# Kernel tuning notes

Measured on AMD Instinct MI355X. Metric: run time of the kernel, lower is better.

The kernel has to match this reference:

```python
import jax, jax.numpy as jnp
import numpy as np

B, S, N, D = 32, 512, 64, 64


def setup_inputs() -> dict:
    key = jax.random.key(0)
    ks = jax.random.split(key, 6)
    return {
        "x": jax.random.normal(ks[0], (B, S, N, D), dtype=jnp.float32),
        "q_embed_weight": jax.random.normal(ks[1], (N, D), dtype=jnp.float32) * 0.02,
        "Wq_w": jax.random.normal(ks[2], (D, D), dtype=jnp.float32) * (1.0 / np.sqrt(D)),
        "Wq_b": jax.random.normal(ks[3], (D,), dtype=jnp.float32) * 0.02,
        "Wkv_w": jax.random.normal(ks[4], (2 * D, D), dtype=jnp.float32) * (1.0 / np.sqrt(D)),
        "Wkv_b": jax.random.normal(ks[5], (2 * D,), dtype=jnp.float32) * 0.02,
    }


def reference(x, q_embed_weight, Wq_w, Wq_b, Wkv_w, Wkv_b):
    d = x.shape[-1]
    # q = Wq(q_embed.weight): [n, d]
    q = q_embed_weight @ Wq_w.T + Wq_b
    # Wkv(x) -> [b, s, n, 2d]; chunk -> k is first half (v half is computed but unused, matching torch)
    kv = jnp.einsum('bsnd,ed->bsne', x, Wkv_w) + Wkv_b
    k = kv[..., :d]
    # prod: full contraction over n and d -> [b, s]
    prod = jnp.einsum('nd,bsnd->bs', q, k) / jnp.sqrt(jnp.asarray(d, x.dtype))
    attn = jax.nn.softmax(prod, axis=1)  # softmax over s
    # weighted sum over s with v = x (original overwrites v): [b, n, d]
    out = jnp.einsum('bs,bsnd->bnd', attn, x)
    return out
```

## Files before the change

kernel.cpp:

```cpp
#include <hip/hip_runtime.h>

#define B_    32
#define S_    512
#define ND_   4096
#define ND4_  1024
#define SCH   16
#define CH    32
#define NPH   (CH/2)
#define NUNIT (B_ * SCH)

typedef float f4 __attribute__((ext_vector_type(4)));
typedef float f2 __attribute__((ext_vector_type(2)));

__global__ void qw_kernel(const float* __restrict__ qe, const float* __restrict__ Wq_w,
                          const float* __restrict__ Wq_b, const float* __restrict__ Wkv_w,
                          float* __restrict__ qw) {
    const int n = blockIdx.x;
    const int t = threadIdx.x;
    __shared__ float qrow[64];
    float acc = Wq_b[t];
    const float* qen = qe + n * 64;
    const float* wqr = Wq_w + t * 64;
#pragma unroll 8
    for (int d = 0; d < 64; ++d) acc += qen[d] * wqr[d];
    qrow[t] = acc;
    __syncthreads();
    float s = 0.f;
#pragma unroll 8
    for (int e = 0; e < 64; ++e) s += qrow[e] * Wkv_w[e * 64 + t];
    qw[n * 64 + t] = s * 0.125f;
}

__global__ __launch_bounds__(256) void flash_partial(
    const float* __restrict__ x, const float* __restrict__ qw,
    float* __restrict__ po, float* __restrict__ pml) {
    const int blk = blockIdx.x;
    const int b   = blk >> 4;
    const int c   = blk & (SCH - 1);
    const int t   = threadIdx.x;
    const int w   = t >> 6;
    const int l   = t & 63;

    __shared__ f2 red[2][4];

    const f4* qw4 = (const f4*)qw;
    f4 qv[4];
#pragma unroll
    for (int k = 0; k < 4; ++k) qv[k] = qw4[k * 256 + t];

    f4 o[4];
#pragma unroll
    for (int k = 0; k < 4; ++k) o[k] = (f4)(0.f);
    float lsum = 0.f;

    const f4* xb = (const f4*)x + (size_t)(b * S_ + c * CH) * ND4_;

    f4 cur[2][4], nxt[2][4];
#pragma unroll
    for (int rr = 0; rr < 2; ++rr)
#pragma unroll
        for (int k = 0; k < 4; ++k) cur[rr][k] = xb[(size_t)rr * ND4_ + k * 256 + t];

    for (int ph = 0; ph < NPH; ++ph) {
        if (ph + 1 < NPH) {
            const f4* xn = xb + (size_t)(2 * ph + 2) * ND4_;
#pragma unroll
            for (int rr = 0; rr < 2; ++rr)
#pragma unroll
                for (int k = 0; k < 4; ++k) nxt[rr][k] = xn[(size_t)rr * ND4_ + k * 256 + t];
        }

        float pd0 = 0.f, pd1 = 0.f;
#pragma unroll
        for (int k = 0; k < 4; ++k) {
            pd0 += cur[0][k][0] * qv[k][0] + cur[0][k][1] * qv[k][1] +
                   cur[0][k][2] * qv[k][2] + cur[0][k][3] * qv[k][3];
            pd1 += cur[1][k][0] * qv[k][0] + cur[1][k][1] * qv[k][1] +
                   cur[1][k][2] * qv[k][2] + cur[1][k][3] * qv[k][3];
        }
#pragma unroll
        for (int off = 32; off > 0; off >>= 1) {
            pd0 += __shfl_xor(pd0, off, 64);
            pd1 += __shfl_xor(pd1, off, 64);
        }

        const int par = ph & 1;
        if (l == 0) { f2 v = { pd0, pd1 }; red[par][w] = v; }
        asm volatile("s_waitcnt lgkmcnt(0)" ::: "memory");
        __builtin_amdgcn_s_barrier();
        __builtin_amdgcn_sched_barrier(0);
        const f2 pr = red[par][0] + red[par][1] + red[par][2] + red[par][3];

        const float e0 = __expf(fminf(pr[0] - 8.f, 52.f));
        const float e1 = __expf(fminf(pr[1] - 8.f, 52.f));
        lsum += e0 + e1;
#pragma unroll
        for (int k = 0; k < 4; ++k) o[k] += e0 * cur[0][k] + e1 * cur[1][k];

        if (ph + 1 < NPH) {
#pragma unroll
            for (int rr = 0; rr < 2; ++rr)
#pragma unroll
                for (int k = 0; k < 4; ++k) cur[rr][k] = nxt[rr][k];
        }
    }

    f4* pob = (f4*)po + (size_t)blk * ND4_;
#pragma unroll
    for (int k = 0; k < 4; ++k) pob[k * 256 + t] = o[k];
    if (t == 0) pml[blk] = lsum;
}

__global__ __launch_bounds__(256) void combine_kernel(
    const float* __restrict__ po, const float* __restrict__ pml,
    float* __restrict__ out) {
    const int b    = blockIdx.x >> 2;
    const int seg  = blockIdx.x & 3;
    const int t    = threadIdx.x;
    const int idx4 = seg * 256 + t;
    __shared__ float sl[SCH];
    if (t < SCH) sl[t] = pml[b * SCH + t];
    __syncthreads();
    float L = 0.f;
    f4 acc = (f4)(0.f);
#pragma unroll
    for (int c = 0; c < SCH; ++c) {
        L   += sl[c];
        acc += ((const f4*)po)[(size_t)(b * SCH + c) * ND4_ + idx4];
    }
    ((f4*)out)[(size_t)b * ND4_ + idx4] = acc * (1.f / L);
}

extern "C" void kernel_launch(void* const* d_in, const int* in_sizes, int n_in,
                              void* d_out, int out_size, void* d_ws, size_t ws_size,
                              hipStream_t stream) {
    const float* x     = (const float*)d_in[0];
    const float* qe    = (const float*)d_in[1];
    const float* Wq_w  = (const float*)d_in[2];
    const float* Wq_b  = (const float*)d_in[3];
    const float* Wkv_w = (const float*)d_in[4];
    float* out = (float*)d_out;

    float* qw  = (float*)d_ws;
    float* pml = qw + ND_;
    float* po  = pml + NUNIT;

    qw_kernel<<<dim3(64), dim3(64), 0, stream>>>(qe, Wq_w, Wq_b, Wkv_w, qw);
    flash_partial<<<dim3(NUNIT), dim3(256), 0, stream>>>(x, qw, po, pml);
    combine_kernel<<<dim3(B_ * 4), dim3(256), 0, stream>>>(po, pml, out);
}
```

Before: 54.73 us.

## Fuse query projection into flash partial kernel, computing it redundantly per block

Removes the separate qw kernel and has every flash_partial block compute the projected query vector itself into shared memory before streaming x. This drops one kernel launch and the dependency gap between the launches. In exchange, each of the 512 blocks repeats the two small 64x64 matmuls, which adds serial prologue latency and extra L2 traffic per block.

```diff
diff --git a/kernel.cpp b/kernel.cpp
--- a/kernel.cpp
+++ b/kernel.cpp
@@ -12,27 +12,10 @@
 typedef float f4 __attribute__((ext_vector_type(4)));
 typedef float f2 __attribute__((ext_vector_type(2)));
 
-__global__ void qw_kernel(const float* __restrict__ qe, const float* __restrict__ Wq_w,
-                          const float* __restrict__ Wq_b, const float* __restrict__ Wkv_w,
-                          float* __restrict__ qw) {
-    const int n = blockIdx.x;
-    const int t = threadIdx.x;
-    __shared__ float qrow[64];
-    float acc = Wq_b[t];
-    const float* qen = qe + n * 64;
-    const float* wqr = Wq_w + t * 64;
-#pragma unroll 8
-    for (int d = 0; d < 64; ++d) acc += qen[d] * wqr[d];
-    qrow[t] = acc;
-    __syncthreads();
-    float s = 0.f;
-#pragma unroll 8
-    for (int e = 0; e < 64; ++e) s += qrow[e] * Wkv_w[e * 64 + t];
-    qw[n * 64 + t] = s * 0.125f;
-}
-
 __global__ __launch_bounds__(256) void flash_partial(
-    const float* __restrict__ x, const float* __restrict__ qw,
+    const float* __restrict__ x, const float* __restrict__ qe,
+    const float* __restrict__ Wq_w, const float* __restrict__ Wq_b,
+    const float* __restrict__ Wkv_w,
     float* __restrict__ po, float* __restrict__ pml) {
     const int blk = blockIdx.x;
     const int b   = blk >> 4;
@@ -41,17 +24,8 @@
     const int w   = t >> 6;
     const int l   = t & 63;
 
+    __shared__ float qlds[64][64];
     __shared__ f2 red[2][4];
-
-    const f4* qw4 = (const f4*)qw;
-    f4 qv[4];
-#pragma unroll
-    for (int k = 0; k < 4; ++k) qv[k] = qw4[k * 256 + t];
-
-    f4 o[4];
-#pragma unroll
-    for (int k = 0; k < 4; ++k) o[k] = (f4)(0.f);
-    float lsum = 0.f;
 
     const f4* xb = (const f4*)x + (size_t)(b * S_ + c * CH) * ND4_;
 
@@ -60,6 +34,43 @@
     for (int rr = 0; rr < 2; ++rr)
 #pragma unroll
         for (int k = 0; k < 4; ++k) cur[rr][k] = xb[(size_t)rr * ND4_ + k * 256 + t];
+
+    {
+        const int n  = t >> 2;
+        const int e0 = (t & 3) * 16;
+        const float* qen = qe + n * 64;
+#pragma unroll
+        for (int ee = 0; ee < 16; ++ee) {
+            const int e = e0 + ee;
+            const float* wqr = Wq_w + e * 64;
+            float a = Wq_b[e];
+#pragma unroll 8
+            for (int d = 0; d < 64; ++d) a += qen[d] * wqr[d];
+            qlds[n][e] = a;
+        }
+    }
+    __syncthreads();
+
+    f4 qv[4];
+    {
+        const int d0 = (4 * t) & 63;
+#pragma unroll
+        for (int k = 0; k < 4; ++k) {
+            const int nk = 16 * k + (t >> 4);
+            f4 a = (f4)(0.f);
+#pragma unroll 8
+            for (int e = 0; e < 64; ++e) {
+                const f4 wv = *(const f4*)(Wkv_w + e * 64 + d0);
+                a += qlds[nk][e] * wv;
+            }
+            qv[k] = a * 0.125f;
+        }
+    }
+
+    f4 o[4];
+#pragma unroll
+    for (int k = 0; k < 4; ++k) o[k] = (f4)(0.f);
+    float lsum = 0.f;
 
     for (int ph = 0; ph < NPH; ++ph) {
         if (ph + 1 < NPH) {
@@ -141,11 +152,9 @@
     const float* Wkv_w = (const float*)d_in[4];
     float* out = (float*)d_out;
 
-    float* qw  = (float*)d_ws;
-    float* pml = qw + ND_;
+    float* pml = (float*)d_ws;
     float* po  = pml + NUNIT;
 
-    qw_kernel<<<dim3(64), dim3(64), 0, stream>>>(qe, Wq_w, Wq_b, Wkv_w, qw);
-    flash_partial<<<dim3(NUNIT), dim3(256), 0, stream>>>(x, qw, po, pml);
+    flash_partial<<<dim3(NUNIT), dim3(256), 0, stream>>>(x, qe, Wq_w, Wq_b, Wkv_w, po, pml);
     combine_kernel<<<dim3(B_ * 4), dim3(256), 0, stream>>>(po, pml, out);
 }
```

Result: slower. 131.7 us (+140.6%).

## Accumulate partial outputs with global atomics and replace combine with divide pass

Applied to the files above, without the earlier changes.

Instead of writing per-chunk partial outputs and summing them in a combine kernel, each block atomically adds its unnormalized numerator and denominator into a per-batch buffer zeroed by the qw kernel. A light divide kernel then normalizes. This removes the partial buffer write and reread, at the cost of many scalar float atomics and a nondeterministic summation order.

```diff
diff --git a/kernel.cpp b/kernel.cpp
--- a/kernel.cpp
+++ b/kernel.cpp
@@ -12,11 +12,21 @@
 typedef float f4 __attribute__((ext_vector_type(4)));
 typedef float f2 __attribute__((ext_vector_type(2)));
 
+#define DEN_OFF (B_ * ND_)
+#define QW_OFF  (DEN_OFF + 64)
+
 __global__ void qw_kernel(const float* __restrict__ qe, const float* __restrict__ Wq_w,
                           const float* __restrict__ Wq_b, const float* __restrict__ Wkv_w,
-                          float* __restrict__ qw) {
+                          float* __restrict__ ws) {
     const int n = blockIdx.x;
     const int t = threadIdx.x;
+    {
+        f4* num4 = (f4*)ws;
+        const int base = n * 64 + t;
+#pragma unroll
+        for (int i = 0; i < 8; ++i) num4[base + i * 4096] = (f4)(0.f);
+        if (n == 0 && t < B_) ws[DEN_OFF + t] = 0.f;
+    }
     __shared__ float qrow[64];
     float acc = Wq_b[t];
     const float* qen = qe + n * 64;
@@ -28,12 +38,15 @@
     float s = 0.f;
 #pragma unroll 8
     for (int e = 0; e < 64; ++e) s += qrow[e] * Wkv_w[e * 64 + t];
-    qw[n * 64 + t] = s * 0.125f;
+    ws[QW_OFF + n * 64 + t] = s * 0.125f;
 }
 
 __global__ __launch_bounds__(256) void flash_partial(
-    const float* __restrict__ x, const float* __restrict__ qw,
-    float* __restrict__ po, float* __restrict__ pml) {
+    const float* __restrict__ x, float* __restrict__ ws) {
+    const float* qw = ws + QW_OFF;
+    float* num = ws;
+    float* den = ws + DEN_OFF;
+
     const int blk = blockIdx.x;
     const int b   = blk >> 4;
     const int c   = blk & (SCH - 1);
@@ -105,30 +118,24 @@
         }
     }
 
-    f4* pob = (f4*)po + (size_t)blk * ND4_;
+    float* nb = num + (size_t)b * ND_;
 #pragma unroll
-    for (int k = 0; k < 4; ++k) pob[k * 256 + t] = o[k];
-    if (t == 0) pml[blk] = lsum;
+    for (int k = 0; k < 4; ++k) {
+        const int e4 = (k * 256 + t) * 4;
+        atomicAdd(nb + e4 + 0, o[k][0]);
+        atomicAdd(nb + e4 + 1, o[k][1]);
+        atomicAdd(nb + e4 + 2, o[k][2]);
+        atomicAdd(nb + e4 + 3, o[k][3]);
+    }
+    if (t == 0) atomicAdd(den + b, lsum);
 }
 
-__global__ __launch_bounds__(256) void combine_kernel(
-    const float* __restrict__ po, const float* __restrict__ pml,
-    float* __restrict__ out) {
-    const int b    = blockIdx.x >> 2;
-    const int seg  = blockIdx.x & 3;
-    const int t    = threadIdx.x;
-    const int idx4 = seg * 256 + t;
-    __shared__ float sl[SCH];
-    if (t < SCH) sl[t] = pml[b * SCH + t];
-    __syncthreads();
-    float L = 0.f;
-    f4 acc = (f4)(0.f);
-#pragma unroll
-    for (int c = 0; c < SCH; ++c) {
-        L   += sl[c];
-        acc += ((const f4*)po)[(size_t)(b * SCH + c) * ND4_ + idx4];
-    }
-    ((f4*)out)[(size_t)b * ND4_ + idx4] = acc * (1.f / L);
+__global__ __launch_bounds__(256) void divide_kernel(
+    const float* __restrict__ ws, float* __restrict__ out) {
+    const int idx4 = blockIdx.x * 256 + threadIdx.x;
+    const int b    = idx4 >> 10;
+    const float inv = 1.f / ws[DEN_OFF + b];
+    ((f4*)out)[idx4] = ((const f4*)ws)[idx4] * inv;
 }
 
 extern "C" void kernel_launch(void* const* d_in, const int* in_sizes, int n_in,
@@ -140,12 +147,9 @@
     const float* Wq_b  = (const float*)d_in[3];
     const float* Wkv_w = (const float*)d_in[4];
     float* out = (float*)d_out;
+    float* ws  = (float*)d_ws;
 
-    float* qw  = (float*)d_ws;
-    float* pml = qw + ND_;
-    float* po  = pml + NUNIT;
-
-    qw_kernel<<<dim3(64), dim3(64), 0, stream>>>(qe, Wq_w, Wq_b, Wkv_w, qw);
-    flash_partial<<<dim3(NUNIT), dim3(256), 0, stream>>>(x, qw, po, pml);
-    combine_kernel<<<dim3(B_ * 4), dim3(256), 0, stream>>>(po, pml, out);
+    qw_kernel<<<dim3(64), dim3(64), 0, stream>>>(qe, Wq_w, Wq_b, Wkv_w, ws);
+    flash_partial<<<dim3(NUNIT), dim3(256), 0, stream>>>(x, ws);
+    divide_kernel<<<dim3(128), dim3(256), 0, stream>>>(ws, out);
 }
```

Measured after the change: 73.59 us. +34.5%, slower.
